# Optimization experiments

Hardware: AMD Instinct MI355X
Metric: run time of the kernel (lower is better)

## Reference

```python
import jax, jax.numpy as jnp
import numpy as np

EMBED = 2048
HEAD = 128

def setup_inputs() -> dict:
    key = jax.random.key(0)
    ks = jax.random.split(key, 7)
    s = 1.0 / np.sqrt(EMBED)
    x = jax.random.normal(ks[0], (8, 2048, EMBED), dtype=jnp.float32)
    Wq = jax.random.uniform(ks[1], (EMBED, HEAD), jnp.float32, -s, s)
    bq = jax.random.uniform(ks[2], (HEAD,), jnp.float32, -s, s)
    Wk = jax.random.uniform(ks[3], (EMBED, HEAD), jnp.float32, -s, s)
    bk = jax.random.uniform(ks[4], (HEAD,), jnp.float32, -s, s)
    Wv = jax.random.uniform(ks[5], (EMBED, HEAD), jnp.float32, -s, s)
    bv = jax.random.uniform(ks[6], (HEAD,), jnp.float32, -s, s)
    return {"x": x, "Wq": Wq, "bq": bq, "Wk": Wk, "bk": bk, "Wv": Wv, "bv": bv}

def reference(x, Wq, bq, Wk, bk, Wv, bv):
    # x: [B, T, E]
    T = x.shape[1]
    Q = x @ Wq + bq  # [B, T, H]
    K = x @ Wk + bk
    V = x @ Wv + bv
    scale = 1.0 / jnp.sqrt(jnp.float32(HEAD))
    scores = jnp.einsum('bqh,bkh->bqk', Q, K) * scale  # [B, T, T]
    causal = jnp.tril(jnp.ones((T, T), dtype=bool))
    scores = jnp.where(causal, scores, jnp.float32(-jnp.inf))
    att = jax.nn.softmax(scores, axis=-1)
    # dropout is identity in eval/reference mode
    return jnp.einsum('bqk,bkh->bqh', att, V)
```

## Files before the change

kernel.cpp:

```cpp
#include <hip/hip_runtime.h>

#define EMBED 2048
#define HEAD 128
#define BATCH 8
#define SEQ 2048

typedef __attribute__((ext_vector_type(4))) float f32x4;
typedef __attribute__((ext_vector_type(8))) __bf16 bf16x8;
typedef __attribute__((ext_vector_type(8))) short short8;

static __device__ __forceinline__ ushort f2bf(float x){
    unsigned u = __float_as_uint(x);
    u += 0x7fffu + ((u >> 16) & 1u);
    return (ushort)(u >> 16);
}

#define MFMA16(a,b,c) __builtin_amdgcn_mfma_f32_16x16x32_bf16((a),(b),(c),0,0,0)

#define GLL16(g, l) __builtin_amdgcn_global_load_lds( \
    (const __attribute__((address_space(1))) void*)(g), \
    (__attribute__((address_space(3))) void*)(l), 16, 0, 0)

__global__ __launch_bounds__(256) void prep_wt(const float* __restrict__ Wq,
                                               const float* __restrict__ Wk,
                                               const float* __restrict__ Wv,
                                               ushort* __restrict__ wt){
    __shared__ float ld[64][129];
    const int w  = blockIdx.y;
    const int k0 = blockIdx.x * 64;
    const int tid = threadIdx.x;
    const float* W = (w == 0) ? Wq : ((w == 1) ? Wk : Wv);
    #pragma unroll
    for (int ii = 0; ii < 32; ii++){
        int idx = tid + 256 * ii;
        int row = idx >> 7, col = idx & 127;
        ld[row][col] = W[(size_t)(k0 + row) * HEAD + col];
    }
    __syncthreads();
    int n  = tid >> 1;
    int kh = (tid & 1) * 32;
    __attribute__((aligned(16))) ushort tmp[32];
    #pragma unroll
    for (int ii = 0; ii < 32; ii++) tmp[ii] = f2bf(ld[kh + ii][n]);
    ushort* dst = wt + (size_t)(w * HEAD + n) * EMBED + k0 + kh;
    #pragma unroll
    for (int q = 0; q < 4; q++)
        *(short8*)(dst + q * 8) = *(const short8*)(tmp + q * 8);
}

__global__ __launch_bounds__(512) void qkv_gemm(const float* __restrict__ x,
                                                const ushort* __restrict__ wt,
                                                const float* __restrict__ bq,
                                                const float* __restrict__ bk,
                                                const float* __restrict__ bv,
                                                ushort* __restrict__ Qb,
                                                ushort* __restrict__ Kb,
                                                ushort* __restrict__ Vt){
    __shared__ char smem[116736];
    float* ts = (float*)smem;

    const int mtile = blockIdx.x;
    const int tid   = threadIdx.x;
    const int lane  = tid & 63;
    const int wid   = tid >> 6;
    const int l15   = lane & 15, lhi = lane >> 4;
    const int wm    = wid >> 2,  wn  = wid & 3;
    const int xrow0 = mtile * 64;

    const int srow = tid >> 3;
    const int ssub = tid & 7;

    const int grow = lane >> 3;
    const int gch  = lane & 7;

    f32x4 acc[2][6];
    #pragma unroll
    for (int i = 0; i < 2; i++)
        #pragma unroll
        for (int j = 0; j < 6; j++) acc[i][j] = (f32x4){0.f,0.f,0.f,0.f};

    float4 xr0, xr1;
    const int NK = EMBED / 64;

    {
        const float* xp = x + (size_t)(xrow0 + srow) * EMBED;
        xr0 = *(const float4*)(xp + ssub * 8);
        xr1 = *(const float4*)(xp + ssub * 8 + 4);
        #pragma unroll
        for (int g = 0; g < 6; g++){
            int r0  = wid * 48 + g * 8;
            int row = r0 + grow;
            GLL16(wt + (size_t)row * EMBED + ((gch ^ grow) * 8), smem + 18432 + r0 * 128);
        }
        __attribute__((aligned(16))) ushort t8[8];
        t8[0]=f2bf(xr0.x); t8[1]=f2bf(xr0.y); t8[2]=f2bf(xr0.z); t8[3]=f2bf(xr0.w);
        t8[4]=f2bf(xr1.x); t8[5]=f2bf(xr1.y); t8[6]=f2bf(xr1.z); t8[7]=f2bf(xr1.w);
        *(short8*)(smem + srow * 144 + ssub * 16) = *(const short8*)t8;
    }
    __syncthreads();

    int cur = 0;
    for (int kt = 0; kt < NK; ++kt){
        char* xsb_c = smem + cur * 9216;
        char* wlb_c = smem + 18432 + cur * 49152;
        char* xsb_n = smem + (cur ^ 1) * 9216;
        char* wlb_n = smem + 18432 + (cur ^ 1) * 49152;
        if (kt < NK - 1){
            const float* xp = x + (size_t)(xrow0 + srow) * EMBED + (kt + 1) * 64;
            xr0 = *(const float4*)(xp + ssub * 8);
            xr1 = *(const float4*)(xp + ssub * 8 + 4);
            const ushort* wsrc = wt + (kt + 1) * 64;
            #pragma unroll
            for (int g = 0; g < 6; g++){
                int r0  = wid * 48 + g * 8;
                int row = r0 + grow;
                GLL16(wsrc + (size_t)row * EMBED + ((gch ^ grow) * 8), wlb_n + r0 * 128);
            }
        }
        #pragma unroll
        for (int kc = 0; kc < 2; kc++){
            bf16x8 af[2], bfj[6];
            #pragma unroll
            for (int i = 0; i < 2; i++)
                af[i] = *(const bf16x8*)(xsb_c + (wm*32 + i*16 + l15) * 144 + kc*64 + lhi*16);
            #pragma unroll
            for (int j = 0; j < 6; j++){
                int row = wn*96 + j*16 + l15;
                bfj[j] = *(const bf16x8*)(wlb_c + row * 128 + (((kc*4 + lhi) ^ (l15 & 7)) * 16));
            }
            #pragma unroll
            for (int i = 0; i < 2; i++)
                #pragma unroll
                for (int j = 0; j < 6; j++)
                    acc[i][j] = MFMA16(af[i], bfj[j], acc[i][j]);
        }
        if (kt < NK - 1){
            __attribute__((aligned(16))) ushort t8[8];
            t8[0]=f2bf(xr0.x); t8[1]=f2bf(xr0.y); t8[2]=f2bf(xr0.z); t8[3]=f2bf(xr0.w);
            t8[4]=f2bf(xr1.x); t8[5]=f2bf(xr1.y); t8[6]=f2bf(xr1.z); t8[7]=f2bf(xr1.w);
            *(short8*)(xsb_n + srow * 144 + ssub * 16) = *(const short8*)t8;
        }
        __syncthreads();
        cur ^= 1;
    }

    float bval[6];
    #pragma unroll
    for (int j = 0; j < 6; j++){
        int c = wn*96 + j*16 + l15;
        bval[j] = (c < 128) ? bq[c] : ((c < 256) ? bk[c - 128] : bv[c - 256]);
    }
    #pragma unroll
    for (int j = 0; j < 6; j++){
        int cb = wn*96 + j*16;
        if (cb < 256){
            ushort* dst = (cb < 128) ? Qb : Kb;
            int cl = (cb & 127) + l15;
            #pragma unroll
            for (int i = 0; i < 2; i++)
                #pragma unroll
                for (int r = 0; r < 4; r++){
                    int m = mtile*64 + wm*32 + i*16 + lhi*4 + r;
                    dst[(size_t)m * HEAD + cl] = f2bf(acc[i][j][r] + bval[j]);
                }
        } else {
            int vc = cb - 256 + l15;
            #pragma unroll
            for (int i = 0; i < 2; i++)
                #pragma unroll
                for (int r = 0; r < 4; r++){
                    int ml = wm*32 + i*16 + lhi*4 + r;
                    ts[ml * 132 + vc] = acc[i][j][r] + bval[j];
                }
        }
    }
    __syncthreads();
    {
        int n  = tid >> 2;
        int mc = (tid & 3) * 16;
        int bb = mtile >> 5;
        int trow = (mtile & 31) * 64 + mc;
        __attribute__((aligned(16))) ushort tmp[16];
        #pragma unroll
        for (int ii = 0; ii < 16; ii++) tmp[ii] = f2bf(ts[(mc + ii) * 132 + n]);
        ushort* dst = Vt + ((size_t)(bb * HEAD + n)) * SEQ + trow;
        *(short8*)(dst)     = *(const short8*)(tmp);
        *(short8*)(dst + 8) = *(const short8*)(tmp + 8);
    }
}

__global__ __launch_bounds__(256) void attn(const ushort* __restrict__ Qb,
                                            const ushort* __restrict__ Kb,
                                            const ushort* __restrict__ Vt,
                                            float* __restrict__ po,
                                            float* __restrict__ pm,
                                            float* __restrict__ pl){
    __shared__ char smem[40960];
    char* Ks = smem;
    char* Vs = smem + 16384;
    char* Ps = smem + 32768;

    const int slot = blockIdx.x;
    const int b    = blockIdx.y;
    const int qi   = slot >> 1;
    const int qt   = (b < 4) ? qi : (31 - qi);
    const int half = slot & 1;
    const int NT   = qt + 1;
    const int tmid = (NT + 1) >> 1;
    const int t0   = half ? tmid : 0;
    const int t1   = half ? NT : tmid;

    const int qb    = qt * 64;
    const int tid   = threadIdx.x;
    const int lane  = tid & 63, wid = tid >> 6;
    const int l15   = lane & 15, lhi = lane >> 4;
    const float scale = 0.08838834764831845f;

    bf16x8 qf[4];
    {
        const ushort* qp = Qb + ((size_t)(b * SEQ + qb + wid * 16 + l15)) * HEAD;
        #pragma unroll
        for (int kc = 0; kc < 4; kc++)
            qf[kc] = *(const bf16x8*)(qp + kc * 32 + lhi * 8);
    }

    f32x4 o[8];
    #pragma unroll
    for (int d = 0; d < 8; d++) o[d] = (f32x4){0.f,0.f,0.f,0.f};
    float mr[4] = {-1e30f,-1e30f,-1e30f,-1e30f};
    float lr[4] = {0.f,0.f,0.f,0.f};

    char* Pw = Ps + wid * 2048;

    const int krow = tid >> 4, kch = tid & 15;
    const int vd   = tid >> 3, vch = tid & 7;

    short8 kr[4], vr[4];
    {
        const int kvb = t0 * 64;
        #pragma unroll
        for (int j = 0; j < 4; j++)
            kr[j] = *(const short8*)(Kb + ((size_t)(b * SEQ + kvb + krow + 16*j)) * HEAD + kch * 8);
        #pragma unroll
        for (int j = 0; j < 4; j++)
            vr[j] = *(const short8*)(Vt + ((size_t)(b * HEAD + vd + 32*j)) * SEQ + kvb + vch * 8);
    }

    for (int t = t0; t < t1; ++t){
        __syncthreads();
        #pragma unroll
        for (int j = 0; j < 4; j++){
            int row = krow + 16*j;
            *(short8*)(Ks + row * 256 + ((kch ^ (row & 15)) * 16)) = kr[j];
        }
        #pragma unroll
        for (int j = 0; j < 4; j++){
            int d = vd + 32*j;
            *(short8*)(Vs + d * 128 + ((vch ^ (d & 7)) * 16)) = vr[j];
        }
        if (t + 1 < t1){
            const int kvb2 = (t + 1) * 64;
            #pragma unroll
            for (int j = 0; j < 4; j++)
                kr[j] = *(const short8*)(Kb + ((size_t)(b * SEQ + kvb2 + krow + 16*j)) * HEAD + kch * 8);
            #pragma unroll
            for (int j = 0; j < 4; j++)
                vr[j] = *(const short8*)(Vt + ((size_t)(b * HEAD + vd + 32*j)) * SEQ + kvb2 + vch * 8);
        }
        asm volatile("s_waitcnt lgkmcnt(0)" ::: "memory");
        __builtin_amdgcn_s_barrier();
        __builtin_amdgcn_sched_barrier(0);

        const int kvb = t * 64;
        f32x4 s[4];
        #pragma unroll
        for (int ns = 0; ns < 4; ns++){
            s[ns] = (f32x4){0.f,0.f,0.f,0.f};
            int row = ns * 16 + l15;
            #pragma unroll
            for (int kc = 0; kc < 4; kc++){
                int ch = (kc * 4 + lhi) ^ (row & 15);
                bf16x8 bfr = *(const bf16x8*)(Ks + row * 256 + ch * 16);
                s[ns] = MFMA16(qf[kc], bfr, s[ns]);
            }
        }

        float mx[4];
        #pragma unroll
        for (int r = 0; r < 4; r++){
            #pragma unroll
            for (int ns = 0; ns < 4; ns++){
                float v = s[ns][r] * scale;
                if (t == qt){
                    int kvg = kvb + ns * 16 + l15;
                    int qg  = qb + wid * 16 + lhi * 4 + r;
                    if (kvg > qg) v = -1e30f;
                }
                s[ns][r] = v;
            }
            float m0 = fmaxf(fmaxf(s[0][r], s[1][r]), fmaxf(s[2][r], s[3][r]));
            m0 = fmaxf(m0, __shfl_xor(m0, 1));
            m0 = fmaxf(m0, __shfl_xor(m0, 2));
            m0 = fmaxf(m0, __shfl_xor(m0, 4));
            m0 = fmaxf(m0, __shfl_xor(m0, 8));
            mx[r] = m0;
        }
        float alpha[4];
        #pragma unroll
        for (int r = 0; r < 4; r++){
            float mn = fmaxf(mr[r], mx[r]);
            alpha[r] = __expf(mr[r] - mn);
            mr[r] = mn;
            float sum = 0.f;
            #pragma unroll
            for (int ns = 0; ns < 4; ns++){
                float p = __expf(s[ns][r] - mn);
                s[ns][r] = p;
                sum += p;
            }
            sum += __shfl_xor(sum, 1);
            sum += __shfl_xor(sum, 2);
            sum += __shfl_xor(sum, 4);
            sum += __shfl_xor(sum, 8);
            lr[r] = lr[r] * alpha[r] + sum;
        }
        #pragma unroll
        for (int d = 0; d < 8; d++)
            #pragma unroll
            for (int r = 0; r < 4; r++) o[d][r] *= alpha[r];

        #pragma unroll
        for (int ns = 0; ns < 4; ns++)
            #pragma unroll
            for (int r = 0; r < 4; r++){
                int row = lhi * 4 + r;
                int byteoff = row * 128 + (((ns * 16 + l15) * 2) ^ ((row & 7) << 4));
                *(ushort*)(Pw + byteoff) = f2bf(s[ns][r]);
            }
        asm volatile("s_waitcnt lgkmcnt(0)" ::: "memory");
        __builtin_amdgcn_sched_barrier(0);

        #pragma unroll
        for (int kc = 0; kc < 2; kc++){
            int abyte = l15 * 128 + ((kc * 64 + lhi * 16) ^ ((l15 & 7) << 4));
            bf16x8 af = *(const bf16x8*)(Pw + abyte);
            #pragma unroll
            for (int ds = 0; ds < 8; ds++){
                int drow = ds * 16 + l15;
                int bbyte = drow * 128 + ((kc * 64 + lhi * 16) ^ ((drow & 7) << 4));
                bf16x8 bfr = *(const bf16x8*)(Vs + bbyte);
                o[ds] = MFMA16(af, bfr, o[ds]);
            }
        }
    }

    float* pob = po + ((size_t)half * 16384 + (size_t)b * SEQ) * HEAD;
    #pragma unroll
    for (int r = 0; r < 4; r++){
        int q = qb + wid * 16 + lhi * 4 + r;
        #pragma unroll
        for (int ds = 0; ds < 8; ds++)
            pob[(size_t)q * HEAD + ds * 16 + l15] = o[ds][r];
        if (l15 == 0){
            pm[half * 16384 + b * SEQ + q] = mr[r];
            pl[half * 16384 + b * SEQ + q] = lr[r];
        }
    }
}

__global__ __launch_bounds__(256) void merge(const float* __restrict__ po,
                                             const float* __restrict__ pm,
                                             const float* __restrict__ pl,
                                             float* __restrict__ out){
    int g = blockIdx.x * 256 + threadIdx.x;
    int row = g >> 2;
    int dq  = (g & 3) * 32;
    float m0 = pm[row], m1 = pm[16384 + row];
    float l0 = pl[row], l1 = pl[16384 + row];
    float M  = fmaxf(m0, m1);
    float w0 = __expf(m0 - M), w1 = __expf(m1 - M);
    float inv = 1.0f / (w0 * l0 + w1 * l1);
    const float4* p0 = (const float4*)(po + (size_t)row * HEAD + dq);
    const float4* p1 = (const float4*)(po + (size_t)(16384 + row) * HEAD + dq);
    float4* op = (float4*)(out + (size_t)row * HEAD + dq);
    #pragma unroll
    for (int i = 0; i < 8; i++){
        float4 a = p0[i], c = p1[i];
        float4 r;
        r.x = (w0*a.x + w1*c.x) * inv;
        r.y = (w0*a.y + w1*c.y) * inv;
        r.z = (w0*a.z + w1*c.z) * inv;
        r.w = (w0*a.w + w1*c.w) * inv;
        op[i] = r;
    }
}

extern "C" void kernel_launch(void* const* d_in, const int* in_sizes, int n_in,
                              void* d_out, int out_size, void* d_ws, size_t ws_size,
                              hipStream_t stream){
    const float* x  = (const float*)d_in[0];
    const float* Wq = (const float*)d_in[1];
    const float* bq = (const float*)d_in[2];
    const float* Wk = (const float*)d_in[3];
    const float* bk = (const float*)d_in[4];
    const float* Wv = (const float*)d_in[5];
    const float* bv = (const float*)d_in[6];
    float* out = (float*)d_out;

    char* ws = (char*)d_ws;
    ushort* Qb = (ushort*)ws;
    ushort* Kb = (ushort*)(ws + (size_t)4  * 1024 * 1024);
    ushort* Vt = (ushort*)(ws + (size_t)8  * 1024 * 1024);
    ushort* Wt = (ushort*)(ws + (size_t)12 * 1024 * 1024);
    float*  po = (float*) (ws + (size_t)14 * 1024 * 1024);
    float*  pm = (float*) (ws + (size_t)31 * 1024 * 1024);
    float*  pl = (float*) (ws + (size_t)31 * 1024 * 1024 + 262144);

    prep_wt <<<dim3(32, 3), 256, 0, stream>>>(Wq, Wk, Wv, Wt);
    qkv_gemm<<<dim3(256), 512, 0, stream>>>(x, Wt, bq, bk, bv, Qb, Kb, Vt);
    attn    <<<dim3(64, 8), 256, 0, stream>>>(Qb, Kb, Vt, po, pm, pl);
    merge   <<<256, 256, 0, stream>>>(po, pm, pl, out);
}
```

Measured before the change: 99.09 us.

## Shrink QKV GEMM tiles to 32 rows, single-buffer LDS, two blocks per CU

The QKV projection kernel now uses 256-thread blocks covering 32 rows instead of 512-thread blocks covering 64 rows, so it launches 512 blocks and fits two per CU. LDS drops from about 114KB to about 52KB by replacing the double buffer with a single buffer. Explicit waitcnt and barrier instructions sequence the loads, and the x register prefetch for the next step still overlaps compute. The weight tile is now reloaded for every 32 rows, which doubles weight traffic, and the weight global-to-LDS load is no longer overlapped with MFMA work inside a block. The design relies on the second resident block to hide that latency.

```diff
diff --git a/kernel.cpp b/kernel.cpp
--- a/kernel.cpp
+++ b/kernel.cpp
@@ -48,15 +48,15 @@
         *(short8*)(dst + q * 8) = *(const short8*)(tmp + q * 8);
 }
 
-__global__ __launch_bounds__(512) void qkv_gemm(const float* __restrict__ x,
-                                                const ushort* __restrict__ wt,
-                                                const float* __restrict__ bq,
-                                                const float* __restrict__ bk,
-                                                const float* __restrict__ bv,
-                                                ushort* __restrict__ Qb,
-                                                ushort* __restrict__ Kb,
-                                                ushort* __restrict__ Vt){
-    __shared__ char smem[116736];
+__global__ __launch_bounds__(256, 2) void qkv_gemm(const float* __restrict__ x,
+                                                   const ushort* __restrict__ wt,
+                                                   const float* __restrict__ bq,
+                                                   const float* __restrict__ bk,
+                                                   const float* __restrict__ bv,
+                                                   ushort* __restrict__ Qb,
+                                                   ushort* __restrict__ Kb,
+                                                   ushort* __restrict__ Vt){
+    __shared__ char smem[53760];
     float* ts = (float*)smem;
 
     const int mtile = blockIdx.x;
@@ -64,8 +64,8 @@
     const int lane  = tid & 63;
     const int wid   = tid >> 6;
     const int l15   = lane & 15, lhi = lane >> 4;
-    const int wm    = wid >> 2,  wn  = wid & 3;
-    const int xrow0 = mtile * 64;
+    const int wn    = wid;
+    const int xrow0 = mtile * 32;
 
     const int srow = tid >> 3;
     const int ssub = tid & 7;
@@ -73,60 +73,59 @@
     const int grow = lane >> 3;
     const int gch  = lane & 7;
 
+    char* xs = smem;
+    char* wl = smem + 4608;
+
     f32x4 acc[2][6];
     #pragma unroll
     for (int i = 0; i < 2; i++)
         #pragma unroll
         for (int j = 0; j < 6; j++) acc[i][j] = (f32x4){0.f,0.f,0.f,0.f};
 
+    const int NK = EMBED / 64;
     float4 xr0, xr1;
-    const int NK = EMBED / 64;
-
     {
         const float* xp = x + (size_t)(xrow0 + srow) * EMBED;
         xr0 = *(const float4*)(xp + ssub * 8);
         xr1 = *(const float4*)(xp + ssub * 8 + 4);
-        #pragma unroll
-        for (int g = 0; g < 6; g++){
-            int r0  = wid * 48 + g * 8;
-            int row = r0 + grow;
-            GLL16(wt + (size_t)row * EMBED + ((gch ^ grow) * 8), smem + 18432 + r0 * 128);
-        }
-        __attribute__((aligned(16))) ushort t8[8];
-        t8[0]=f2bf(xr0.x); t8[1]=f2bf(xr0.y); t8[2]=f2bf(xr0.z); t8[3]=f2bf(xr0.w);
-        t8[4]=f2bf(xr1.x); t8[5]=f2bf(xr1.y); t8[6]=f2bf(xr1.z); t8[7]=f2bf(xr1.w);
-        *(short8*)(smem + srow * 144 + ssub * 16) = *(const short8*)t8;
-    }
-    __syncthreads();
-
-    int cur = 0;
+    }
+
     for (int kt = 0; kt < NK; ++kt){
-        char* xsb_c = smem + cur * 9216;
-        char* wlb_c = smem + 18432 + cur * 49152;
-        char* xsb_n = smem + (cur ^ 1) * 9216;
-        char* wlb_n = smem + 18432 + (cur ^ 1) * 49152;
+        {
+            __attribute__((aligned(16))) ushort t8[8];
+            t8[0]=f2bf(xr0.x); t8[1]=f2bf(xr0.y); t8[2]=f2bf(xr0.z); t8[3]=f2bf(xr0.w);
+            t8[4]=f2bf(xr1.x); t8[5]=f2bf(xr1.y); t8[6]=f2bf(xr1.z); t8[7]=f2bf(xr1.w);
+            *(short8*)(xs + srow * 144 + ssub * 16) = *(const short8*)t8;
+        }
+        {
+            const ushort* wsrc = wt + kt * 64;
+            #pragma unroll
+            for (int g = 0; g < 12; g++){
+                int r0  = wid * 96 + g * 8;
+                int row = r0 + grow;
+                GLL16(wsrc + (size_t)row * EMBED + ((gch ^ grow) * 8), wl + r0 * 128);
+            }
+        }
         if (kt < NK - 1){
             const float* xp = x + (size_t)(xrow0 + srow) * EMBED + (kt + 1) * 64;
             xr0 = *(const float4*)(xp + ssub * 8);
             xr1 = *(const float4*)(xp + ssub * 8 + 4);
-            const ushort* wsrc = wt + (kt + 1) * 64;
-            #pragma unroll
-            for (int g = 0; g < 6; g++){
-                int r0  = wid * 48 + g * 8;
-                int row = r0 + grow;
-                GLL16(wsrc + (size_t)row * EMBED + ((gch ^ grow) * 8), wlb_n + r0 * 128);
-            }
-        }
+        }
+        asm volatile("s_waitcnt lgkmcnt(0)" ::: "memory");
+        if (kt < NK - 1) asm volatile("s_waitcnt vmcnt(2)" ::: "memory");
+        else             asm volatile("s_waitcnt vmcnt(0)" ::: "memory");
+        __builtin_amdgcn_s_barrier();
+
         #pragma unroll
         for (int kc = 0; kc < 2; kc++){
             bf16x8 af[2], bfj[6];
             #pragma unroll
             for (int i = 0; i < 2; i++)
-                af[i] = *(const bf16x8*)(xsb_c + (wm*32 + i*16 + l15) * 144 + kc*64 + lhi*16);
+                af[i] = *(const bf16x8*)(xs + (i*16 + l15) * 144 + kc*64 + lhi*16);
             #pragma unroll
             for (int j = 0; j < 6; j++){
                 int row = wn*96 + j*16 + l15;
-                bfj[j] = *(const bf16x8*)(wlb_c + row * 128 + (((kc*4 + lhi) ^ (l15 & 7)) * 16));
+                bfj[j] = *(const bf16x8*)(wl + row * 128 + (((kc*4 + lhi) ^ (l15 & 7)) * 16));
             }
             #pragma unroll
             for (int i = 0; i < 2; i++)
@@ -134,14 +133,7 @@
                 for (int j = 0; j < 6; j++)
                     acc[i][j] = MFMA16(af[i], bfj[j], acc[i][j]);
         }
-        if (kt < NK - 1){
-            __attribute__((aligned(16))) ushort t8[8];
-            t8[0]=f2bf(xr0.x); t8[1]=f2bf(xr0.y); t8[2]=f2bf(xr0.z); t8[3]=f2bf(xr0.w);
-            t8[4]=f2bf(xr1.x); t8[5]=f2bf(xr1.y); t8[6]=f2bf(xr1.z); t8[7]=f2bf(xr1.w);
-            *(short8*)(xsb_n + srow * 144 + ssub * 16) = *(const short8*)t8;
-        }
-        __syncthreads();
-        cur ^= 1;
+        __builtin_amdgcn_s_barrier();
     }
 
     float bval[6];
@@ -160,26 +152,32 @@
             for (int i = 0; i < 2; i++)
                 #pragma unroll
                 for (int r = 0; r < 4; r++){
-                    int m = mtile*64 + wm*32 + i*16 + lhi*4 + r;
+                    int m = mtile*32 + i*16 + lhi*4 + r;
                     dst[(size_t)m * HEAD + cl] = f2bf(acc[i][j][r] + bval[j]);
                 }
-        } else {
+        }
+    }
+    __syncthreads();
+    #pragma unroll
+    for (int j = 0; j < 6; j++){
+        int cb = wn*96 + j*16;
+        if (cb >= 256){
             int vc = cb - 256 + l15;
             #pragma unroll
             for (int i = 0; i < 2; i++)
                 #pragma unroll
                 for (int r = 0; r < 4; r++){
-                    int ml = wm*32 + i*16 + lhi*4 + r;
+                    int ml = i*16 + lhi*4 + r;
                     ts[ml * 132 + vc] = acc[i][j][r] + bval[j];
                 }
         }
     }
     __syncthreads();
     {
-        int n  = tid >> 2;
-        int mc = (tid & 3) * 16;
-        int bb = mtile >> 5;
-        int trow = (mtile & 31) * 64 + mc;
+        int n  = tid >> 1;
+        int mc = (tid & 1) * 16;
+        int bb = mtile >> 6;
+        int trow = (mtile & 63) * 32 + mc;
         __attribute__((aligned(16))) ushort tmp[16];
         #pragma unroll
         for (int ii = 0; ii < 16; ii++) tmp[ii] = f2bf(ts[(mc + ii) * 132 + n]);
@@ -417,7 +415,7 @@
     float*  pl = (float*) (ws + (size_t)31 * 1024 * 1024 + 262144);
 
     prep_wt <<<dim3(32, 3), 256, 0, stream>>>(Wq, Wk, Wv, Wt);
-    qkv_gemm<<<dim3(256), 512, 0, stream>>>(x, Wt, bq, bk, bv, Qb, Kb, Vt);
+    qkv_gemm<<<dim3(512), 256, 0, stream>>>(x, Wt, bq, bk, bv, Qb, Kb, Vt);
     attn    <<<dim3(64, 8), 256, 0, stream>>>(Qb, Kb, Vt, po, pm, pl);
     merge   <<<256, 256, 0, stream>>>(po, pm, pl, out);
 }
```

Measured after the change: 100.7 us. No clear change (+1.6%).

## Load QKV weight fragments directly from global memory instead of staging through LDS

Applied to the files above, without the earlier changes.

The QKV projection GEMM stops staging the transposed bf16 weight tile in shared memory and has each wave read its own B fragments straight from global memory. The wave layout changes so each wave owns 48 output columns across all 64 rows. Shared memory drops from about 114 KB to 33 KB, and launch bounds now request 4 blocks per SM to raise occupancy. In exchange, the weight loads are no longer prefetched a stage ahead and their latency lands directly in the MFMA loop, relying on L2 hits and the extra occupancy to hide it.

```diff
diff --git a/kernel.cpp b/kernel.cpp
--- a/kernel.cpp
+++ b/kernel.cpp
@@ -16,10 +16,6 @@
 }
 
 #define MFMA16(a,b,c) __builtin_amdgcn_mfma_f32_16x16x32_bf16((a),(b),(c),0,0,0)
-
-#define GLL16(g, l) __builtin_amdgcn_global_load_lds( \
-    (const __attribute__((address_space(1))) void*)(g), \
-    (__attribute__((address_space(3))) void*)(l), 16, 0, 0)
 
 __global__ __launch_bounds__(256) void prep_wt(const float* __restrict__ Wq,
                                                const float* __restrict__ Wk,
@@ -48,15 +44,15 @@
         *(short8*)(dst + q * 8) = *(const short8*)(tmp + q * 8);
 }
 
-__global__ __launch_bounds__(512) void qkv_gemm(const float* __restrict__ x,
-                                                const ushort* __restrict__ wt,
-                                                const float* __restrict__ bq,
-                                                const float* __restrict__ bk,
-                                                const float* __restrict__ bv,
-                                                ushort* __restrict__ Qb,
-                                                ushort* __restrict__ Kb,
-                                                ushort* __restrict__ Vt){
-    __shared__ char smem[116736];
+__global__ __launch_bounds__(512, 4) void qkv_gemm(const float* __restrict__ x,
+                                                   const ushort* __restrict__ wt,
+                                                   const float* __restrict__ bq,
+                                                   const float* __restrict__ bk,
+                                                   const float* __restrict__ bv,
+                                                   ushort* __restrict__ Qb,
+                                                   ushort* __restrict__ Kb,
+                                                   ushort* __restrict__ Vt){
+    __shared__ char smem[33792];
     float* ts = (float*)smem;
 
     const int mtile = blockIdx.x;
@@ -64,34 +60,27 @@
     const int lane  = tid & 63;
     const int wid   = tid >> 6;
     const int l15   = lane & 15, lhi = lane >> 4;
-    const int wm    = wid >> 2,  wn  = wid & 3;
     const int xrow0 = mtile * 64;
 
     const int srow = tid >> 3;
     const int ssub = tid & 7;
 
-    const int grow = lane >> 3;
-    const int gch  = lane & 7;
-
-    f32x4 acc[2][6];
-    #pragma unroll
-    for (int i = 0; i < 2; i++)
-        #pragma unroll
-        for (int j = 0; j < 6; j++) acc[i][j] = (f32x4){0.f,0.f,0.f,0.f};
-
+    const ushort* wb0 = wt + (size_t)(wid * 48 +  0 + l15) * EMBED + lhi * 8;
+    const ushort* wb1 = wt + (size_t)(wid * 48 + 16 + l15) * EMBED + lhi * 8;
+    const ushort* wb2 = wt + (size_t)(wid * 48 + 32 + l15) * EMBED + lhi * 8;
+
+    f32x4 acc[4][3];
+    #pragma unroll
+    for (int i = 0; i < 4; i++)
+        #pragma unroll
+        for (int j = 0; j < 3; j++) acc[i][j] = (f32x4){0.f,0.f,0.f,0.f};
+
+    const int NK = EMBED / 64;
     float4 xr0, xr1;
-    const int NK = EMBED / 64;
-
     {
         const float* xp = x + (size_t)(xrow0 + srow) * EMBED;
         xr0 = *(const float4*)(xp + ssub * 8);
         xr1 = *(const float4*)(xp + ssub * 8 + 4);
-        #pragma unroll
-        for (int g = 0; g < 6; g++){
-            int r0  = wid * 48 + g * 8;
-            int row = r0 + grow;
-            GLL16(wt + (size_t)row * EMBED + ((gch ^ grow) * 8), smem + 18432 + r0 * 128);
-        }
         __attribute__((aligned(16))) ushort t8[8];
         t8[0]=f2bf(xr0.x); t8[1]=f2bf(xr0.y); t8[2]=f2bf(xr0.z); t8[3]=f2bf(xr0.w);
         t8[4]=f2bf(xr1.x); t8[5]=f2bf(xr1.y); t8[6]=f2bf(xr1.z); t8[7]=f2bf(xr1.w);
@@ -99,77 +88,71 @@
     }
     __syncthreads();
 
-    int cur = 0;
     for (int kt = 0; kt < NK; ++kt){
-        char* xsb_c = smem + cur * 9216;
-        char* wlb_c = smem + 18432 + cur * 49152;
-        char* xsb_n = smem + (cur ^ 1) * 9216;
-        char* wlb_n = smem + 18432 + (cur ^ 1) * 49152;
+        char* xs_c = smem + (kt & 1) * 9216;
+        char* xs_n = smem + ((kt + 1) & 1) * 9216;
         if (kt < NK - 1){
             const float* xp = x + (size_t)(xrow0 + srow) * EMBED + (kt + 1) * 64;
             xr0 = *(const float4*)(xp + ssub * 8);
             xr1 = *(const float4*)(xp + ssub * 8 + 4);
-            const ushort* wsrc = wt + (kt + 1) * 64;
-            #pragma unroll
-            for (int g = 0; g < 6; g++){
-                int r0  = wid * 48 + g * 8;
-                int row = r0 + grow;
-                GLL16(wsrc + (size_t)row * EMBED + ((gch ^ grow) * 8), wlb_n + r0 * 128);
-            }
         }
         #pragma unroll
         for (int kc = 0; kc < 2; kc++){
-            bf16x8 af[2], bfj[6];
-            #pragma unroll
-            for (int i = 0; i < 2; i++)
-                af[i] = *(const bf16x8*)(xsb_c + (wm*32 + i*16 + l15) * 144 + kc*64 + lhi*16);
-            #pragma unroll
-            for (int j = 0; j < 6; j++){
-                int row = wn*96 + j*16 + l15;
-                bfj[j] = *(const bf16x8*)(wlb_c + row * 128 + (((kc*4 + lhi) ^ (l15 & 7)) * 16));
-            }
-            #pragma unroll
-            for (int i = 0; i < 2; i++)
+            const int ko = kt * 64 + kc * 32;
+            bf16x8 af[4], bfj[3];
+            bfj[0] = *(const bf16x8*)(wb0 + ko);
+            bfj[1] = *(const bf16x8*)(wb1 + ko);
+            bfj[2] = *(const bf16x8*)(wb2 + ko);
+            #pragma unroll
+            for (int i = 0; i < 4; i++)
+                af[i] = *(const bf16x8*)(xs_c + (i*16 + l15) * 144 + kc*64 + lhi*16);
+            #pragma unroll
+            for (int i = 0; i < 4; i++)
                 #pragma unroll
-                for (int j = 0; j < 6; j++)
+                for (int j = 0; j < 3; j++)
                     acc[i][j] = MFMA16(af[i], bfj[j], acc[i][j]);
         }
         if (kt < NK - 1){
             __attribute__((aligned(16))) ushort t8[8];
             t8[0]=f2bf(xr0.x); t8[1]=f2bf(xr0.y); t8[2]=f2bf(xr0.z); t8[3]=f2bf(xr0.w);
             t8[4]=f2bf(xr1.x); t8[5]=f2bf(xr1.y); t8[6]=f2bf(xr1.z); t8[7]=f2bf(xr1.w);
-            *(short8*)(xsb_n + srow * 144 + ssub * 16) = *(const short8*)t8;
+            *(short8*)(xs_n + srow * 144 + ssub * 16) = *(const short8*)t8;
         }
         __syncthreads();
-        cur ^= 1;
-    }
-
-    float bval[6];
-    #pragma unroll
-    for (int j = 0; j < 6; j++){
-        int c = wn*96 + j*16 + l15;
+    }
+
+    float bval[3];
+    #pragma unroll
+    for (int j = 0; j < 3; j++){
+        int c = wid*48 + j*16 + l15;
         bval[j] = (c < 128) ? bq[c] : ((c < 256) ? bk[c - 128] : bv[c - 256]);
     }
     #pragma unroll
-    for (int j = 0; j < 6; j++){
-        int cb = wn*96 + j*16;
+    for (int j = 0; j < 3; j++){
+        int cb = wid*48 + j*16;
         if (cb < 256){
             ushort* dst = (cb < 128) ? Qb : Kb;
             int cl = (cb & 127) + l15;
             #pragma unroll
-            for (int i = 0; i < 2; i++)
+            for (int i = 0; i < 4; i++)
                 #pragma unroll
                 for (int r = 0; r < 4; r++){
-                    int m = mtile*64 + wm*32 + i*16 + lhi*4 + r;
+                    int m = mtile*64 + i*16 + lhi*4 + r;
                     dst[(size_t)m * HEAD + cl] = f2bf(acc[i][j][r] + bval[j]);
                 }
-        } else {
+        }
+    }
+    __syncthreads();
+    #pragma unroll
+    for (int j = 0; j < 3; j++){
+        int cb = wid*48 + j*16;
+        if (cb >= 256){
             int vc = cb - 256 + l15;
             #pragma unroll
-            for (int i = 0; i < 2; i++)
+            for (int i = 0; i < 4; i++)
                 #pragma unroll
                 for (int r = 0; r < 4; r++){
-                    int ml = wm*32 + i*16 + lhi*4 + r;
+                    int ml = i*16 + lhi*4 + r;
                     ts[ml * 132 + vc] = acc[i][j][r] + bval[j];
                 }
         }
```

Result: slower. 119.4 us (+20.5%).
